# Kernel optimization log

Measured on AMD Instinct MI355X. Metric: run time of the kernel, lower is better.

The kernel has to match this reference:

```python
import jax, jax.numpy as jnp
import numpy as np
from math import sqrt

L, H, D, HD, F, V, P = 8, 16, 1024, 64, 4096, 32000, 2048
B, S = 2, 2048
EPS = 1e-5


def _ln(x, g, b):
    m = jnp.mean(x, axis=-1, keepdims=True)
    v = jnp.mean((x - m) ** 2, axis=-1, keepdims=True)
    return (x - m) * jax.lax.rsqrt(v + EPS) * g + b


def setup_inputs() -> dict:
    key = jax.random.key(0)
    ks = jax.random.split(key, 12)
    w = 0.02
    return {
        'input_ids': jax.random.randint(ks[0], (B, S), 0, V),
        'tok_emb': jax.random.normal(ks[1], (V, D), jnp.float32) * w,
        'pos_emb': jax.random.normal(ks[2], (P, D), jnp.float32) * w,
        'emb_g': jnp.ones((D,), jnp.float32),
        'emb_b': jnp.zeros((D,), jnp.float32),
        'ln1_g': jnp.ones((L, D), jnp.float32),
        'ln1_b': jnp.zeros((L, D), jnp.float32),
        'ln2_g': jnp.ones((L, D), jnp.float32),
        'ln2_b': jnp.zeros((L, D), jnp.float32),
        'Wq': jax.random.normal(ks[3], (L, H, D, HD), jnp.float32) * w,
        'bq': jnp.zeros((L, H, HD), jnp.float32),
        'Wk': jax.random.normal(ks[4], (L, H, D, HD), jnp.float32) * w,
        'bk': jnp.zeros((L, H, HD), jnp.float32),
        'Wv': jax.random.normal(ks[5], (L, H, D, HD), jnp.float32) * w,
        'bv': jnp.zeros((L, H, HD), jnp.float32),
        'Wo': jax.random.normal(ks[6], (L, D, D), jnp.float32) * w,
        'bo': jnp.zeros((L, D), jnp.float32),
        'W1': jax.random.normal(ks[7], (L, D, F), jnp.float32) * w,
        'b1': jnp.zeros((L, F), jnp.float32),
        'W2': jax.random.normal(ks[8], (L, F, D), jnp.float32) * w,
        'b2': jnp.zeros((L, D), jnp.float32),
    }


def _encoder(input_ids, tok_emb, pos_emb, emb_g, emb_b, ln1_g, ln1_b, ln2_g,
             ln2_b, Wq, bq, Wk, bk, Wv, bv, Wo, bo, W1, b1, W2, b2):
    seq = input_ids.shape[-1]
    x = tok_emb[input_ids] + pos_emb[:seq][None, :, :]  # [B,S,D]
    x = _ln(x, emb_g, emb_b)  # dropout = identity (eval)

    scale = 1.0 / sqrt(HD)

    def layer(x, p):
        (g1, b1_, g2, b2_, wq, bq_, wk, bk_, wv, bv_, wo, bo_, w1, bb1, w2, bb2) = p
        h = _ln(x, g1, b1_)
        q = jnp.einsum('bsd,hdk->bhsk', h, wq) + bq_[:, None, :]
        k = jnp.einsum('bsd,hdk->bhsk', h, wk) + bk_[:, None, :]
        v = jnp.einsum('bsd,hdk->bhsk', h, wv) + bv_[:, None, :]
        scores = jnp.einsum('bhsk,bhtk->bhst', q, k) * scale
        w = jax.nn.softmax(scores, axis=-1)
        av = jnp.einsum('bhst,bhtk->bhsk', w, v)  # [B,H,S,hd]
        av = jnp.transpose(av, (0, 2, 1, 3)).reshape(x.shape[0], x.shape[1], D)
        x = x + jnp.einsum('bsd,de->bse', av, wo) + bo_
        h2 = _ln(x, g2, b2_)
        f = jax.nn.gelu(jnp.einsum('bsd,df->bsf', h2, w1) + bb1, approximate=False)
        x = x + jnp.einsum('bsf,fd->bsd', f, w2) + bb2
        return x, None

    xs = (ln1_g, ln1_b, ln2_g, ln2_b, Wq, bq, Wk, bk, Wv, bv, Wo, bo, W1, b1, W2, b2)
    x, _ = jax.lax.scan(layer, x, xs)
    return x


def reference(input_ids, tok_emb, pos_emb, emb_g, emb_b, ln1_g, ln1_b, ln2_g,
              ln2_b, Wq, bq, Wk, bk, Wv, bv, Wo, bo, W1, b1, W2, b2):
    return _encoder(input_ids, tok_emb, pos_emb, emb_g, emb_b, ln1_g, ln1_b,
                    ln2_g, ln2_b, Wq, bq, Wk, bk, Wv, bv, Wo, bo, W1, b1, W2, b2)
```

## Files before the change

### kernel.cpp

```cpp
#include <hip/hip_runtime.h>
#include <hip/hip_bf16.h>

#define L_ 8
#define H_ 16
#define D_ 1024
#define HD_ 64
#define F_ 4096
#define B_ 2
#define S_ 2048
#define NTOK (B_*S_)

typedef unsigned short u16;
typedef __bf16 bf16x8 __attribute__((ext_vector_type(8)));
typedef float f32x4 __attribute__((ext_vector_type(4)));

__device__ __forceinline__ u16 f2b(float f){ union{float f; unsigned u;} c; c.f = f; unsigned u = c.u; return (u16)((u + 0x7fffu + ((u>>16)&1u)) >> 16); }
__device__ __forceinline__ u16 f2b_fast(float f){ union{float f; unsigned u;} c; c.f = f; return (u16)((c.u + 0x8000u) >> 16); }
__device__ __forceinline__ float b2f(u16 x){ union{unsigned u; float f;} c; c.u = ((unsigned)x)<<16; return c.f; }

__device__ __forceinline__ void gload16(const u16* g, u16* l){
  __builtin_amdgcn_global_load_lds(
      (const __attribute__((address_space(1))) void*)g,
      (__attribute__((address_space(3))) void*)l,
      16 , 0 , 0 );
}

__device__ __forceinline__ void lds_fence(){
  asm volatile("s_waitcnt lgkmcnt(0)" ::: "memory");
  __builtin_amdgcn_sched_barrier(0);
}

#define WAITV_BAR(n) do { \
  asm volatile("s_waitcnt vmcnt(%0)" :: "i"(n) : "memory"); \
  __builtin_amdgcn_sched_barrier(0); \
  __builtin_amdgcn_s_barrier(); \
} while(0)

__device__ __forceinline__ void blk_reduce2(float& a, float& b, float* sm){
  for (int off=32; off>0; off>>=1){ a += __shfl_down(a,off); b += __shfl_down(b,off); }
  int w = threadIdx.x>>6, ln = threadIdx.x&63;
  if (ln==0){ sm[w]=a; sm[4+w]=b; }
  __syncthreads();
  a = sm[0]+sm[1]+sm[2]+sm[3];
  b = sm[4]+sm[5]+sm[6]+sm[7];
}

__global__ __launch_bounds__(256) void embed_ln(const int* __restrict__ ids,
    const float* __restrict__ tok, const float* __restrict__ pos,
    const float* __restrict__ g, const float* __restrict__ bb,
    float* __restrict__ x)
{
  __shared__ float sm[8];
  int row = blockIdx.x;
  int s   = row % S_;
  int id  = ids[row];
  int d0  = threadIdx.x*4;
  float4 t4 = *(const float4*)(tok + (size_t)id*D_ + d0);
  float4 p4 = *(const float4*)(pos + (size_t)s *D_ + d0);
  float4 v; v.x=t4.x+p4.x; v.y=t4.y+p4.y; v.z=t4.z+p4.z; v.w=t4.w+p4.w;
  float sum = (v.x+v.y)+(v.z+v.w);
  float sq  = v.x*v.x+v.y*v.y+v.z*v.z+v.w*v.w;
  blk_reduce2(sum, sq, sm);
  float mean = sum * (1.0f/D_);
  float var  = sq  * (1.0f/D_) - mean*mean;
  float inv  = rsqrtf(var + 1e-5f);
  float4 g4 = *(const float4*)(g + d0);
  float4 b4 = *(const float4*)(bb + d0);
  float4 o; o.x=(v.x-mean)*inv*g4.x+b4.x; o.y=(v.y-mean)*inv*g4.y+b4.y;
            o.z=(v.z-mean)*inv*g4.z+b4.z; o.w=(v.w-mean)*inv*g4.w+b4.w;
  *(float4*)(x + (size_t)row*D_ + d0) = o;
}

__global__ __launch_bounds__(256) void ln_f32_bf16(const float* __restrict__ x,
    const float* __restrict__ g, const float* __restrict__ bb, u16* __restrict__ out)
{
  __shared__ float sm[8];
  int row = blockIdx.x;
  int d0  = threadIdx.x*4;
  float4 v = *(const float4*)(x + (size_t)row*D_ + d0);
  float sum = (v.x+v.y)+(v.z+v.w);
  float sq  = v.x*v.x+v.y*v.y+v.z*v.z+v.w*v.w;
  blk_reduce2(sum, sq, sm);
  float mean = sum * (1.0f/D_);
  float var  = sq  * (1.0f/D_) - mean*mean;
  float inv  = rsqrtf(var + 1e-5f);
  float4 g4 = *(const float4*)(g + d0);
  float4 b4 = *(const float4*)(bb + d0);
  uint2 w;
  w.x = (unsigned)f2b((v.x-mean)*inv*g4.x+b4.x) | ((unsigned)f2b((v.y-mean)*inv*g4.y+b4.y)<<16);
  w.y = (unsigned)f2b((v.z-mean)*inv*g4.z+b4.z) | ((unsigned)f2b((v.w-mean)*inv*g4.w+b4.w)<<16);
  *(uint2*)(out + (size_t)row*D_ + d0) = w;
}

__global__ __launch_bounds__(256) void repack_all(
    const float* __restrict__ Wq, const float* __restrict__ Wk, const float* __restrict__ Wv,
    const float* __restrict__ Wo, const float* __restrict__ W1, const float* __restrict__ W2,
    u16* __restrict__ wqkvt, u16* __restrict__ wot, u16* __restrict__ w1t, u16* __restrict__ w2t,
    int layer)
{
  __shared__ u16 tile[64*64];
  const int n = blockIdx.x;
  const float* src; u16* dst; int R, C, bx, by;
  if (n < 768){
    int z = n >> 4, xt = n & 15;
    int which = z >> 4, h = z & 15;
    const float* W = (which==0) ? Wq : (which==1) ? Wk : Wv;
    src = W + ((size_t)(layer*H_ + h))*D_*HD_;
    dst = wqkvt + (size_t)(which*1024 + h*64)*D_;
    R = 1024; C = 64; bx = 0; by = xt;
  } else if (n < 1024){
    int q = n - 768;  bx = q & 15; by = q >> 4;
    src = Wo + (size_t)layer*D_*D_;  dst = wot;  R = 1024; C = 1024;
  } else if (n < 2048){
    int q = n - 1024; bx = q & 63; by = q >> 6;
    src = W1 + (size_t)layer*D_*F_;  dst = w1t;  R = 1024; C = 4096;
  } else {
    int q = n - 2048; bx = q & 15; by = q >> 4;
    src = W2 + (size_t)layer*F_*D_;  dst = w2t;  R = 4096; C = 1024;
  }
  int c0 = bx*64, r0 = by*64;
  int t = threadIdx.x;
  #pragma unroll
  for (int i=0;i<2;i++){
    int idx = t + i*256;
    int row = idx>>3, c8 = idx&7;
    const float* p = src + (size_t)(r0+row)*C + c0 + c8*8;
    float4 a = *(const float4*)p;
    float4 b = *(const float4*)(p+4);
    u16 tmp[8];
    tmp[0]=f2b(a.x); tmp[1]=f2b(a.y); tmp[2]=f2b(a.z); tmp[3]=f2b(a.w);
    tmp[4]=f2b(b.x); tmp[5]=f2b(b.y); tmp[6]=f2b(b.z); tmp[7]=f2b(b.w);
    int sw = (row&7) ^ ((row>>3)&7);
    *(uint4*)(&tile[row*64 + ((c8 ^ sw)<<3)]) = *(uint4*)tmp;
  }
  __syncthreads();
  #pragma unroll
  for (int i=0;i<2;i++){
    int idx = t + i*256;
    int oc = idx>>3, tc = idx&7;
    u16 tmp[8];
    #pragma unroll
    for (int j=0;j<8;j++){
      int rr = tc*8 + j;
      int sw = (rr&7) ^ ((rr>>3)&7);
      tmp[j] = tile[rr*64 + ((((oc>>3) ^ sw)<<3) | (oc&7))];
    }
    *(uint4*)(dst + (size_t)(c0+oc)*R + r0 + tc*8) = *(uint4*)tmp;
  }
}

__device__ __forceinline__ void epi_store(float v0,float v1,float v2,float v3,
    float* xres, u16* obf, size_t idx, int epi)
{
  if (epi==1){
    float4 t = *(float4*)(xres + idx);
    t.x += v0; t.y += v1; t.z += v2; t.w += v3;
    *(float4*)(xres + idx) = t;
  } else {
    if (epi==2){
      #define GELU_T(v) { float t2=(v)*(v); float u=(v)*fmaf(t2,0.044715f,1.0f); \
                          float e=exp2f(u*-2.3022082f); (v)=(v)*__builtin_amdgcn_rcpf(1.0f+e); }
      GELU_T(v0); GELU_T(v1); GELU_T(v2); GELU_T(v3);
      #undef GELU_T
    }
    uint2 w;
    w.x = (unsigned)f2b_fast(v0) | ((unsigned)f2b_fast(v1) << 16);
    w.y = (unsigned)f2b_fast(v2) | ((unsigned)f2b_fast(v3) << 16);
    *(uint2*)(obf + idx) = w;
  }
}

__global__ __launch_bounds__(256) void gemm_64x128(
    const u16* __restrict__ A, const u16* __restrict__ Bt,
    const float* __restrict__ bias0, float* __restrict__ xres,
    int M, int N, int K)
{
  __shared__ u16 As[64*64];
  __shared__ u16 Bs[128*64];
  const int tid = threadIdx.x;
  const int nbx = gridDim.x;
  const int nwg = nbx * gridDim.y;
  int bid = blockIdx.x + nbx*blockIdx.y;
  int nid = (bid & 7)*(nwg >> 3) + (bid >> 3);
  const int bm = (nid % nbx) * 64;
  const int bn = (nid / nbx) * 128;
  const int wv = tid>>6, ln = tid&63;
  const int wr = wv>>1, wc = wv&1;
  const int l15 = ln&15, lhi = ln>>4;
  const int l8 = ln>>3;
  const int c8s = (ln&7) ^ l8;
  f32x4 acc[2][4];
  const f32x4 zero4 = {0.f,0.f,0.f,0.f};
  #pragma unroll
  for (int i=0;i<2;i++)
    #pragma unroll
    for (int j=0;j<4;j++) acc[i][j] = zero4;

  for (int k0 = 0; k0 < K; k0 += 64) {
    #pragma unroll
    for (int i=0;i<2;i++){
      int row = wv*16 + i*8 + l8;
      gload16(A + (size_t)(bm+row)*K + k0 + c8s*8, &As[(wv*16 + i*8)*64]);
    }
    #pragma unroll
    for (int i=0;i<4;i++){
      int row = wv*32 + i*8 + l8;
      gload16(Bt + (size_t)(bn+row)*K + k0 + c8s*8, &Bs[(wv*32 + i*8)*64]);
    }
    __syncthreads();
    #pragma unroll
    for (int ks=0; ks<2; ks++){
      bf16x8 af[2], bfr[4];
      #pragma unroll
      for (int i=0;i<2;i++){
        int ra = wr*32 + i*16 + l15;
        af[i]  = *(const bf16x8*)(&As[ra*64 + (((ks*4+lhi) ^ (ra&7))<<3)]);
      }
      #pragma unroll
      for (int j=0;j<4;j++){
        int rb = wc*64 + j*16 + l15;
        bfr[j] = *(const bf16x8*)(&Bs[rb*64 + (((ks*4+lhi) ^ (rb&7))<<3)]);
      }
      #pragma unroll
      for (int i=0;i<2;i++)
        #pragma unroll
        for (int j=0;j<4;j++)
          acc[i][j] = __builtin_amdgcn_mfma_f32_16x16x32_bf16(bfr[j], af[i], acc[i][j], 0,0,0);
    }
    __syncthreads();
  }

  #pragma unroll
  for (int j=0;j<4;j++){
    int col0 = bn + wc*64 + j*16 + lhi*4;
    float4 bv4 = *(const float4*)(bias0 + col0);
    #pragma unroll
    for (int i=0;i<2;i++){
      int row = bm + wr*32 + i*16 + l15;
      size_t idx = (size_t)row*N + col0;
      float4 t = *(float4*)(xres + idx);
      t.x += acc[i][j][0] + bv4.x;
      t.y += acc[i][j][1] + bv4.y;
      t.z += acc[i][j][2] + bv4.z;
      t.w += acc[i][j][3] + bv4.w;
      *(float4*)(xres + idx) = t;
    }
  }
}

__global__ __launch_bounds__(512,2) void gemm256(
    const u16* __restrict__ A, const u16* __restrict__ Bt,
    const float* __restrict__ bias0, const float* __restrict__ bias1, const float* __restrict__ bias2,
    float* __restrict__ xres, u16* __restrict__ obf, u16* __restrict__ vTout,
    int M, int N, int K, int epi)
{
  __shared__ u16 As[2][256*64];
  __shared__ u16 Bs[2][256*64];
  const int tid = threadIdx.x;
  const int nbx = gridDim.x;
  const int nwg = nbx * gridDim.y;
  int bid = blockIdx.x + nbx*blockIdx.y;
  int nid = (bid & 7)*(nwg >> 3) + (bid >> 3);
  const int bm = (nid % nbx) * 256;
  const int bn = (nid / nbx) * 256;
  const int wv = tid>>6, ln = tid&63;
  const int wm = wv>>2, wn = wv&3;
  const int l15 = ln&15, lhi = ln>>4;
  const int l8 = ln>>3;
  const int c8s = (ln&7) ^ l8;

  f32x4 acc[2][2][4][2];
  const f32x4 zero4 = {0.f,0.f,0.f,0.f};
  #pragma unroll
  for (int a=0;a<2;a++)
    #pragma unroll
    for (int b=0;b<2;b++)
      #pragma unroll
      for (int i=0;i<4;i++)
        #pragma unroll
        for (int j=0;j<2;j++) acc[a][b][i][j] = zero4;

  const u16* aB0 = A  + (size_t)(bm + wv*16 + l8)*K + c8s*8;
  const u16* bB0 = Bt + (size_t)(bn + wv*16 + l8)*K + c8s*8;

  #define ISSUE(c, kt) do {                                                  \
    const u16* aB = aB0 + (size_t)(kt)*64;                                   \
    const u16* bB = bB0 + (size_t)(kt)*64;                                   \
    gload16(aB,                 &As[c][(wv*16      )*64]);                   \
    gload16(aB + (size_t)8*K,   &As[c][(wv*16 +   8)*64]);                   \
    gload16(bB,                 &Bs[c][(wv*16      )*64]);                   \
    gload16(bB + (size_t)8*K,   &Bs[c][(wv*16 +   8)*64]);                   \
    gload16(bB + (size_t)128*K, &Bs[c][(128 + wv*16    )*64]);               \
    gload16(bB + (size_t)136*K, &Bs[c][(128 + wv*16 + 8)*64]);               \
    gload16(aB + (size_t)128*K, &As[c][(128 + wv*16    )*64]);               \
    gload16(aB + (size_t)136*K, &As[c][(128 + wv*16 + 8)*64]);               \
  } while(0)

  #define READ_B(c) do {                                                     \
    _Pragma("unroll")                                                        \
    for (int qc=0;qc<2;qc++)                                                 \
      _Pragma("unroll")                                                      \
      for (int j=0;j<2;j++){                                                 \
        int rb = qc*128 + wn*32 + j*16 + l15;                                \
        _Pragma("unroll")                                                    \
        for (int ks=0;ks<2;ks++)                                             \
          bfr[qc][j][ks] = *(const bf16x8*)(&Bs[c][rb*64 + (((ks*4+lhi) ^ (rb&7))<<3)]); \
      }                                                                      \
  } while(0)

  #define READ_A(c, qr) do {                                                 \
    _Pragma("unroll")                                                        \
    for (int i=0;i<4;i++){                                                   \
      int ra = (qr)*128 + wm*64 + i*16 + l15;                                \
      _Pragma("unroll")                                                      \
      for (int ks=0;ks<2;ks++)                                               \
        af[i][ks] = *(const bf16x8*)(&As[c][ra*64 + (((ks*4+lhi) ^ (ra&7))<<3)]); \
    }                                                                        \
  } while(0)

  #define MFMA_Q(qr) do {                                                    \
    __builtin_amdgcn_s_setprio(1);                                           \
    _Pragma("unroll")                                                        \
    for (int ks=0;ks<2;ks++)                                                 \
      _Pragma("unroll")                                                      \
      for (int i=0;i<4;i++)                                                  \
        _Pragma("unroll")                                                    \
        for (int qc=0;qc<2;qc++)                                             \
          _Pragma("unroll")                                                  \
          for (int j=0;j<2;j++)                                              \
            acc[qr][qc][i][j] = __builtin_amdgcn_mfma_f32_16x16x32_bf16(     \
                bfr[qc][j][ks], af[i][ks], acc[qr][qc][i][j], 0,0,0);        \
    __builtin_amdgcn_s_setprio(0);                                           \
  } while(0)

  const int nt = K >> 6;
  ISSUE(0, 0);
  WAITV_BAR(2);
  for (int t=0; t<nt-1; ++t){
    int c = t&1;
    ISSUE(c^1, t+1);
    bf16x8 bfr[2][2][2], af[4][2];
    READ_B(c);
    READ_A(c, 0);
    MFMA_Q(0);
    WAITV_BAR(8);
    READ_A(c, 1);
    MFMA_Q(1);
    WAITV_BAR(2);
  }
  {
    int c = (nt-1)&1;
    bf16x8 bfr[2][2][2], af[4][2];
    READ_B(c);
    READ_A(c, 0);
    MFMA_Q(0);
    WAITV_BAR(0);
    READ_A(c, 1);
    MFMA_Q(1);
  }
  #undef ISSUE
  #undef READ_B
  #undef READ_A
  #undef MFMA_Q

  #pragma unroll
  for (int qc=0; qc<2; qc++)
    #pragma unroll
    for (int j=0;j<2;j++){
      int colbase = bn + qc*128;
      int col0 = colbase + wn*32 + j*16 + lhi*4;
      float4 bv4;
      if (bias1){
        const float* bp = (col0 < 1024) ? (bias0 + col0)
                        : (col0 < 2048) ? (bias1 + col0 - 1024)
                                        : (bias2 + col0 - 2048);
        bv4 = *(const float4*)bp;
      } else {
        bv4 = *(const float4*)(bias0 + col0);
      }
      #pragma unroll
      for (int qr=0; qr<2; qr++)
        #pragma unroll
        for (int i=0;i<4;i++){
          int row = bm + qr*128 + wm*64 + i*16 + l15;
          float v0 = acc[qr][qc][i][j][0]+bv4.x;
          float v1 = acc[qr][qc][i][j][1]+bv4.y;
          float v2 = acc[qr][qc][i][j][2]+bv4.z;
          float v3 = acc[qr][qc][i][j][3]+bv4.w;
          if (vTout && colbase >= 2048){
            int vcol = col0 - 2048;
            int hh = vcol >> 6, hd0 = vcol & 63;
            int bb_ = row >> 11, tk = row & (S_-1);
            u16* vd = vTout + ((size_t)((bb_*16 + hh)*64 + hd0))*S_ + tk;
            vd[0]        = f2b_fast(v0);
            vd[S_]       = f2b_fast(v1);
            vd[2*S_]     = f2b_fast(v2);
            vd[3*(size_t)S_] = f2b_fast(v3);
          } else {
            epi_store(v0, v1, v2, v3, xres, obf, (size_t)row*N + col0, epi);
          }
        }
    }
}

__global__ __launch_bounds__(256) void attn_fwd(const u16* __restrict__ qkv,
    const u16* __restrict__ vT, u16* __restrict__ att)
{
  __shared__ u16 Ks[3][64*64];
  __shared__ u16 Vs[3][64*64];
  __shared__ u16 Ps[4][2][16*64];
  const int tid = threadIdx.x, wv = tid>>6, ln = tid&63, l15 = ln&15, lhi = ln>>4;
  const int l8 = ln>>3;
  const int cs = (ln&7) ^ l8;
  int bid = blockIdx.x + 16*(blockIdx.y + 16*blockIdx.z);
  int nid = (bid & 7)*64 + (bid >> 3);
  const int qt = nid & 15, h = (nid >> 4) & 15, b = nid >> 8;
  const u16* qg = qkv + (size_t)b*S_*3072 + h*64;
  const u16* kg = qg + 1024;
  const u16* vtg = vT + ((size_t)(b*16 + h)*64)*S_;

  bf16x8 qfA[2], qfB[2];
  {
    const u16* qrA = qg + (size_t)(qt*128 + wv*32 + l15)*3072;
    const u16* qrB = qrA + (size_t)16*3072;
    u16 ta[16], tb[16];
    *(uint4*)(ta)   = *(const uint4*)(qrA + lhi*8);
    *(uint4*)(ta+8) = *(const uint4*)(qrA + 32 + lhi*8);
    *(uint4*)(tb)   = *(const uint4*)(qrB + lhi*8);
    *(uint4*)(tb+8) = *(const uint4*)(qrB + 32 + lhi*8);
    #pragma unroll
    for (int i=0;i<16;i++){ ta[i] = f2b_fast(b2f(ta[i]) * 0.18033688f);
                            tb[i] = f2b_fast(b2f(tb[i]) * 0.18033688f); }
    qfA[0] = *(const bf16x8*)(ta); qfA[1] = *(const bf16x8*)(ta+8);
    qfB[0] = *(const bf16x8*)(tb); qfB[1] = *(const bf16x8*)(tb+8);
  }
  const f32x4 zero4 = {0.f,0.f,0.f,0.f};
  f32x4 oaccA[4], oaccB[4];
  #pragma unroll
  for (int j=0;j<4;j++){ oaccA[j] = zero4; oaccB[j] = zero4; }
  float lsumA = 0.f, lsumB = 0.f;

  const int qsw = (l15&7)<<3;
  u16* PsA = &Ps[wv][0][l15*64];
  u16* PsB = &Ps[wv][1][l15*64];

  #define STAGE_KV(bufi, kti) do {                                            \
    _Pragma("unroll")                                                         \
    for (int i_=0;i_<2;i_++){                                                 \
      int r0_ = wv*8 + i_*32;                                                 \
      int row_ = r0_ + l8;                                                    \
      gload16(kg  + (size_t)((kti)*64+row_)*3072 + cs*8, &Ks[bufi][r0_*64]);  \
      gload16(vtg + (size_t)row_*S_ + (kti)*64 + cs*8,   &Vs[bufi][r0_*64]);  \
    }                                                                         \
  } while(0)

  STAGE_KV(0, 0);
  STAGE_KV(1, 1);
  WAITV_BAR(4);
  int cur = 0;

  const int NT = S_/64;
  for (int kt=0; kt<NT; kt++){
    int nxt2 = cur + 2; if (nxt2 >= 3) nxt2 -= 3;
    if (kt+2 < NT) STAGE_KV(nxt2, kt+2);

    f32x4 sA[4], sB[4];
    __builtin_amdgcn_s_setprio(1);
    #pragma unroll
    for (int j=0;j<4;j++){
      sA[j] = zero4; sB[j] = zero4;
      #pragma unroll
      for (int ks=0; ks<2; ks++){
        int kr = j*16 + l15;
        bf16x8 kf = *(const bf16x8*)(&Ks[cur][kr*64 + (((ks*4+lhi) ^ (kr&7))<<3)]);
        sA[j] = __builtin_amdgcn_mfma_f32_16x16x32_bf16(kf, qfA[ks], sA[j], 0,0,0);
        sB[j] = __builtin_amdgcn_mfma_f32_16x16x32_bf16(kf, qfB[ks], sB[j], 0,0,0);
      }
    }
    __builtin_amdgcn_s_setprio(0);

    float partA = 0.f, partB = 0.f;
    #pragma unroll
    for (int j=0;j<4;j++){
      float a0 = exp2f(sA[j][0]), a1 = exp2f(sA[j][1]), a2 = exp2f(sA[j][2]), a3 = exp2f(sA[j][3]);
      float b0 = exp2f(sB[j][0]), b1 = exp2f(sB[j][1]), b2 = exp2f(sB[j][2]), b3 = exp2f(sB[j][3]);
      partA += (a0+a1)+(a2+a3);
      partB += (b0+b1)+(b2+b3);
      unsigned wA0, wA1, wB0, wB1;
      asm("v_cvt_pk_bf16_f32 %0, %1, %2" : "=v"(wA0) : "v"(a0), "v"(a1));
      asm("v_cvt_pk_bf16_f32 %0, %1, %2" : "=v"(wA1) : "v"(a2), "v"(a3));
      asm("v_cvt_pk_bf16_f32 %0, %1, %2" : "=v"(wB0) : "v"(b0), "v"(b1));
      asm("v_cvt_pk_bf16_f32 %0, %1, %2" : "=v"(wB1) : "v"(b2), "v"(b3));
      int e0 = (j*16 + lhi*4) ^ qsw;
      uint2 wa; wa.x = wA0; wa.y = wA1;
      uint2 wb; wb.x = wB0; wb.y = wB1;
      *(uint2*)(PsA + e0) = wa;
      *(uint2*)(PsB + e0) = wb;
    }
    lsumA += partA; lsumB += partB;

    lds_fence();

    bf16x8 pfA[2], pfB[2];
    pfA[0] = *(const bf16x8*)(PsA + ((lhi     ^ (l15&7))<<3));
    pfA[1] = *(const bf16x8*)(PsA + (((4+lhi) ^ (l15&7))<<3));
    pfB[0] = *(const bf16x8*)(PsB + ((lhi     ^ (l15&7))<<3));
    pfB[1] = *(const bf16x8*)(PsB + (((4+lhi) ^ (l15&7))<<3));

    __builtin_amdgcn_s_setprio(1);
    #pragma unroll
    for (int dj=0; dj<4; dj++){
      #pragma unroll
      for (int ks=0; ks<2; ks++){
        int vr = dj*16 + l15;
        bf16x8 vf = *(const bf16x8*)(&Vs[cur][vr*64 + (((ks*4+lhi) ^ (vr&7))<<3)]);
        oaccA[dj] = __builtin_amdgcn_mfma_f32_16x16x32_bf16(pfA[ks], vf, oaccA[dj], 0,0,0);
        oaccB[dj] = __builtin_amdgcn_mfma_f32_16x16x32_bf16(pfB[ks], vf, oaccB[dj], 0,0,0);
      }
    }
    __builtin_amdgcn_s_setprio(0);

    if (kt+2 < NT) { WAITV_BAR(4); }
    else           { WAITV_BAR(0); }
    cur = (cur==2) ? 0 : cur+1;
  }
  #undef STAGE_KV

  float totA = lsumA + __shfl_xor(lsumA, 16); totA += __shfl_xor(totA, 32);
  float totB = lsumB + __shfl_xor(lsumB, 16); totB += __shfl_xor(totB, 32);
  float invA[4], invB[4];
  #pragma unroll
  for (int r=0;r<4;r++){
    invA[r] = __builtin_amdgcn_rcpf(__shfl(totA, lhi*4+r));
    invB[r] = __builtin_amdgcn_rcpf(__shfl(totB, lhi*4+r));
  }

  #pragma unroll
  for (int dj=0; dj<4; dj++){
    #pragma unroll
    for (int r=0;r<4;r++){
      int q = lhi*4 + r;
      int tokA = qt*128 + wv*32 + q;
      int tokB = tokA + 16;
      att[(size_t)(b*S_ + tokA)*D_ + h*HD_ + dj*16 + l15] = f2b_fast(oaccA[dj][r] * invA[r]);
      att[(size_t)(b*S_ + tokB)*D_ + h*HD_ + dj*16 + l15] = f2b_fast(oaccB[dj][r] * invB[r]);
    }
  }
}

extern "C" void kernel_launch(void* const* d_in, const int* in_sizes, int n_in,
                              void* d_out, int out_size, void* d_ws, size_t ws_size,
                              hipStream_t stream)
{
  const int*   ids   = (const int*)d_in[0];
  const float* tok   = (const float*)d_in[1];
  const float* pos   = (const float*)d_in[2];
  const float* emb_g = (const float*)d_in[3];
  const float* emb_b = (const float*)d_in[4];
  const float* ln1g  = (const float*)d_in[5];
  const float* ln1b  = (const float*)d_in[6];
  const float* ln2g  = (const float*)d_in[7];
  const float* ln2b  = (const float*)d_in[8];
  const float* Wq = (const float*)d_in[9];
  const float* bq = (const float*)d_in[10];
  const float* Wk = (const float*)d_in[11];
  const float* bk = (const float*)d_in[12];
  const float* Wv = (const float*)d_in[13];
  const float* bv = (const float*)d_in[14];
  const float* Wo = (const float*)d_in[15];
  const float* bo = (const float*)d_in[16];
  const float* W1 = (const float*)d_in[17];
  const float* b1 = (const float*)d_in[18];
  const float* W2 = (const float*)d_in[19];
  const float* b2 = (const float*)d_in[20];

  float* x = (float*)d_out;
  char* ws = (char*)d_ws;
  u16* h     = (u16*)(ws);
  u16* qkvb  = (u16*)(ws + 8388608);
  u16* att   = (u16*)(ws + 33554432);
  u16* fbuf  = (u16*)(ws + 41943040);
  u16* vT    = fbuf;
  u16* wqkvt = (u16*)(ws + 75497472);
  u16* wot   = (u16*)(ws + 81788928);
  u16* w1t   = (u16*)(ws + 83886080);
  u16* w2t   = (u16*)(ws + 92274688);

  embed_ln<<<NTOK, 256, 0, stream>>>(ids, tok, pos, emb_g, emb_b, x);

  for (int l=0; l<L_; l++){
    ln_f32_bf16<<<NTOK, 256, 0, stream>>>(x, ln1g + l*D_, ln1b + l*D_, h);
    repack_all<<<3072, 256, 0, stream>>>(Wq, Wk, Wv,
        Wo, W1, W2, wqkvt, wot, w1t, w2t, l);
    gemm256<<<dim3(16,12), 512, 0, stream>>>(h, wqkvt,
        bq + l*1024, bk + l*1024, bv + l*1024,
        nullptr, qkvb, vT, NTOK, 3072, 1024, 0);
    attn_fwd<<<dim3(S_/128, H_, B_), 256, 0, stream>>>(qkvb, vT, att);
    gemm_64x128<<<dim3(64,8), 256, 0, stream>>>(att, wot,
        bo + l*D_, x, NTOK, 1024, 1024);
    ln_f32_bf16<<<NTOK, 256, 0, stream>>>(x, ln2g + l*D_, ln2b + l*D_, h);
    gemm256<<<dim3(16,16), 512, 0, stream>>>(h, w1t,
        b1 + l*F_, nullptr, nullptr,
        nullptr, fbuf, nullptr, NTOK, 4096, 1024, 2);
    gemm_64x128<<<dim3(64,8), 256, 0, stream>>>(fbuf, w2t,
        b2 + l*D_, x, NTOK, 1024, 4096);
  }
}
```

Before: 2.098 ms.

## Split attention over two key halves with a separate combine kernel

The attention kernel now splits each query tile's key range into two halves, which doubles the number of blocks. Each half writes an unnormalized bf16 partial output and per-row exp-sums to workspace. A new combine kernel adds the two partials and normalizes by the summed denominators. The aim is more parallelism and occupancy in attention, at the cost of an extra launch, extra global-memory traffic and an added bf16 rounding of the partial outputs. The combine step works only because the existing softmax keeps no running max that would need rescaling.

```diff
diff --git a/kernel.cpp b/kernel.cpp
--- a/kernel.cpp
+++ b/kernel.cpp
@@ -403,8 +403,10 @@
     }
 }
 
-__global__ __launch_bounds__(256) void attn_fwd(const u16* __restrict__ qkv,
-    const u16* __restrict__ vT, u16* __restrict__ att)
+__global__ __launch_bounds__(256) void attn_part(const u16* __restrict__ qkv,
+    const u16* __restrict__ vT,
+    u16* __restrict__ OpA, u16* __restrict__ OpB,
+    float* __restrict__ lpA, float* __restrict__ lpB)
 {
   __shared__ u16 Ks[3][64*64];
   __shared__ u16 Vs[3][64*64];
@@ -412,9 +414,10 @@
   const int tid = threadIdx.x, wv = tid>>6, ln = tid&63, l15 = ln&15, lhi = ln>>4;
   const int l8 = ln>>3;
   const int cs = (ln&7) ^ l8;
-  int bid = blockIdx.x + 16*(blockIdx.y + 16*blockIdx.z);
-  int nid = (bid & 7)*64 + (bid >> 3);
-  const int qt = nid & 15, h = (nid >> 4) & 15, b = nid >> 8;
+  int bid = blockIdx.x + 32*(blockIdx.y + 16*blockIdx.z);
+  int nid = (bid & 7)*128 + (bid >> 3);
+  const int half = nid & 1;
+  const int qt = (nid >> 1) & 15, h = (nid >> 5) & 15, b = nid >> 9;
   const u16* qg = qkv + (size_t)b*S_*3072 + h*64;
   const u16* kg = qg + 1024;
   const u16* vtg = vT + ((size_t)(b*16 + h)*64)*S_;
@@ -454,15 +457,15 @@
     }                                                                         \
   } while(0)
 
-  STAGE_KV(0, 0);
-  STAGE_KV(1, 1);
+  const int kbase = half*16;
+  STAGE_KV(0, kbase+0);
+  STAGE_KV(1, kbase+1);
   WAITV_BAR(4);
   int cur = 0;
 
-  const int NT = S_/64;
-  for (int kt=0; kt<NT; kt++){
+  for (int kti=0; kti<16; kti++){
     int nxt2 = cur + 2; if (nxt2 >= 3) nxt2 -= 3;
-    if (kt+2 < NT) STAGE_KV(nxt2, kt+2);
+    if (kti+2 < 16) STAGE_KV(nxt2, kbase+kti+2);
 
     f32x4 sA[4], sB[4];
     __builtin_amdgcn_s_setprio(1);
@@ -520,19 +523,22 @@
     }
     __builtin_amdgcn_s_setprio(0);
 
-    if (kt+2 < NT) { WAITV_BAR(4); }
-    else           { WAITV_BAR(0); }
+    if (kti+2 < 16) { WAITV_BAR(4); }
+    else            { WAITV_BAR(0); }
     cur = (cur==2) ? 0 : cur+1;
   }
   #undef STAGE_KV
 
   float totA = lsumA + __shfl_xor(lsumA, 16); totA += __shfl_xor(totA, 32);
   float totB = lsumB + __shfl_xor(lsumB, 16); totB += __shfl_xor(totB, 32);
-  float invA[4], invB[4];
-  #pragma unroll
-  for (int r=0;r<4;r++){
-    invA[r] = __builtin_amdgcn_rcpf(__shfl(totA, lhi*4+r));
-    invB[r] = __builtin_amdgcn_rcpf(__shfl(totB, lhi*4+r));
+
+  u16*   Op = half ? OpB : OpA;
+  float* lp = half ? lpB : lpA;
+
+  if (lhi == 0){
+    int tokA = qt*128 + wv*32 + l15;
+    lp[(size_t)(b*S_ + tokA)*16 + h]        = totA;
+    lp[(size_t)(b*S_ + tokA + 16)*16 + h]   = totB;
   }
 
   #pragma unroll
@@ -542,10 +548,32 @@
       int q = lhi*4 + r;
       int tokA = qt*128 + wv*32 + q;
       int tokB = tokA + 16;
-      att[(size_t)(b*S_ + tokA)*D_ + h*HD_ + dj*16 + l15] = f2b_fast(oaccA[dj][r] * invA[r]);
-      att[(size_t)(b*S_ + tokB)*D_ + h*HD_ + dj*16 + l15] = f2b_fast(oaccB[dj][r] * invB[r]);
-    }
-  }
+      Op[(size_t)(b*S_ + tokA)*D_ + h*HD_ + dj*16 + l15] = f2b_fast(oaccA[dj][r]);
+      Op[(size_t)(b*S_ + tokB)*D_ + h*HD_ + dj*16 + l15] = f2b_fast(oaccB[dj][r]);
+    }
+  }
+}
+
+__global__ __launch_bounds__(256) void attn_combine(
+    const u16* __restrict__ OA, const u16* __restrict__ OB,
+    const float* __restrict__ lA, const float* __restrict__ lB,
+    u16* __restrict__ att)
+{
+  int tok = blockIdx.x;
+  int c0 = threadIdx.x*4;
+  int h = c0 >> 6;
+  float l = lA[(size_t)tok*16 + h] + lB[(size_t)tok*16 + h];
+  float inv = __builtin_amdgcn_rcpf(l);
+  uint2 a2 = *(const uint2*)(OA + (size_t)tok*1024 + c0);
+  uint2 b2 = *(const uint2*)(OB + (size_t)tok*1024 + c0);
+  float a0 = b2f((u16)(a2.x)), a1 = b2f((u16)(a2.x>>16));
+  float a2v= b2f((u16)(a2.y)), a3 = b2f((u16)(a2.y>>16));
+  float c0v= b2f((u16)(b2.x)), c1 = b2f((u16)(b2.x>>16));
+  float c2 = b2f((u16)(b2.y)), c3 = b2f((u16)(b2.y>>16));
+  uint2 w;
+  w.x = (unsigned)f2b_fast((a0+c0v)*inv) | ((unsigned)f2b_fast((a1+c1)*inv)<<16);
+  w.y = (unsigned)f2b_fast((a2v+c2)*inv) | ((unsigned)f2b_fast((a3+c3)*inv)<<16);
+  *(uint2*)(att + (size_t)tok*1024 + c0) = w;
 }
 
 extern "C" void kernel_launch(void* const* d_in, const int* in_sizes, int n_in,
@@ -581,6 +609,10 @@
   u16* att   = (u16*)(ws + 33554432);
   u16* fbuf  = (u16*)(ws + 41943040);
   u16* vT    = fbuf;
+  u16* OpA   = (u16*)(ws + 50331648);
+  u16* OpB   = (u16*)(ws + 58720256);
+  float* lpA = (float*)(ws + 67108864);
+  float* lpB = (float*)(ws + 67371008);
   u16* wqkvt = (u16*)(ws + 75497472);
   u16* wot   = (u16*)(ws + 81788928);
   u16* w1t   = (u16*)(ws + 83886080);
@@ -595,7 +627,8 @@
     gemm256<<<dim3(16,12), 512, 0, stream>>>(h, wqkvt,
         bq + l*1024, bk + l*1024, bv + l*1024,
         nullptr, qkvb, vT, NTOK, 3072, 1024, 0);
-    attn_fwd<<<dim3(S_/128, H_, B_), 256, 0, stream>>>(qkvb, vT, att);
+    attn_part<<<dim3(32,16,2), 256, 0, stream>>>(qkvb, vT, OpA, OpB, lpA, lpB);
+    attn_combine<<<NTOK, 256, 0, stream>>>(OpA, OpB, lpA, lpB, att);
     gemm_64x128<<<dim3(64,8), 256, 0, stream>>>(att, wot,
         bo + l*D_, x, NTOK, 1024, 1024);
     ln_f32_bf16<<<NTOK, 256, 0, stream>>>(x, ln2g + l*D_, ln2b + l*D_, h);
```

Result: slower. 2.172 ms (+3.6%).
